# Kernel optimization log

Measured on AMD Instinct MI355X. Metric: run time of the kernel, lower is better.

The kernel has to match this reference:

```python
import jax, jax.numpy as jnp
import numpy as np

NB = 8            # num_blocks
BS = 96           # block_size = hidden_size // num_blocks
HSF = 1           # hidden_size_factor
LAM = 0.01        # sparsity_threshold (softshrink lambda)
FRAC = 1.0        # hard_thresholding_fraction
SCALE = 0.02


def setup_inputs() -> dict:
    key = jax.random.key(0)
    ks = jax.random.split(key, 9)
    B, C, H, W, D = 2, NB * BS, 32, 32, 32
    x = jax.random.normal(ks[0], (B, C, H, W, D), jnp.float32)
    # complex params stored as separate real/imag float arrays (torch.rand on cfloat
    # fills real and imag independently with U[0,1))
    w1r = SCALE * jax.random.uniform(ks[1], (NB, BS, BS * HSF), jnp.float32)
    w1i = SCALE * jax.random.uniform(ks[2], (NB, BS, BS * HSF), jnp.float32)
    w2r = SCALE * jax.random.uniform(ks[3], (NB, BS, BS * HSF), jnp.float32)
    w2i = SCALE * jax.random.uniform(ks[4], (NB, BS, BS * HSF), jnp.float32)
    b1r = SCALE * jax.random.uniform(ks[5], (NB, BS * HSF), jnp.float32)
    b1i = SCALE * jax.random.uniform(ks[6], (NB, BS * HSF), jnp.float32)
    b2r = SCALE * jax.random.uniform(ks[7], (NB, BS), jnp.float32)
    b2i = SCALE * jax.random.uniform(ks[8], (NB, BS), jnp.float32)
    return {"x": x, "w1r": w1r, "w1i": w1i, "w2r": w2r, "w2i": w2i,
            "b1r": b1r, "b1i": b1i, "b2r": b2r, "b2i": b2i}


def _softshrink(v, lam):
    return jnp.sign(v) * jnp.maximum(jnp.abs(v) - lam, 0.0)


def _gelu_c(z):
    # torch GELU applied to view_as_real => separately on real and imag parts
    return jax.nn.gelu(jnp.real(z), approximate=False) + 1j * jax.nn.gelu(jnp.imag(z), approximate=False)


def reference(x, w1r, w1i, w2r, w2i, b1r, b1i, b2r, b2i):
    bias = x
    B, C, H, W, D = x.shape
    w1 = w1r + 1j * w1i
    w2 = w2r + 1j * w2i
    b1 = b1r + 1j * b1i
    b2 = b2r + 1j * b2i

    xf = jnp.fft.rfftn(x.astype(jnp.float32), axes=(-3, -2, -1), norm='ortho')
    Dr = xf.shape[-1]                      # D//2 + 1
    xf = xf.reshape(B, NB, BS, H, W, Dr)

    total_modes = H * W * D // 2 + 1
    kept = min(int(total_modes * FRAC), Dr)  # original slices only the last freq axis
    xk = xf[..., :kept]                      # (B, nb, bs, H, W, kept)

    # block-diagonal complex GEMM 1 + bias, then GELU on real/imag parts
    h1 = jnp.einsum('bnihwd,nio->bnohwd', xk, w1) + b1[None, :, :, None, None, None]
    h1 = _gelu_c(h1)
    # block-diagonal complex GEMM 2 + bias
    h2 = jnp.einsum('bnihwd,nio->bnohwd', h1, w2) + b2[None, :, :, None, None, None]

    # scatter back into full spectrum (zeros beyond kept modes)
    if kept < Dr:
        h2 = jnp.pad(h2, ((0, 0), (0, 0), (0, 0), (0, 0), (0, 0), (0, Dr - kept)))

    # softshrink on real/imag parts
    z = _softshrink(jnp.real(h2), LAM) + 1j * _softshrink(jnp.imag(h2), LAM)
    z = z.reshape(B, C, H, W, Dr)
    out = jnp.fft.irfftn(z, s=(H, W, D), axes=(-3, -2, -1), norm='ortho')
    return out.astype(x.dtype) + bias
```

## Files before the change

kernel.cpp:

```cpp
#include <hip/hip_runtime.h>
#include <math.h>


#define CH    768
#define DR    17
#define PLANE 544
#define NVOL  49152
#define CSTRIDE 17408
#define ORTHO 0.0055242717280199026f
#define TWOPI_32 0.19634954084936207f

typedef __bf16 bf16x8 __attribute__((ext_vector_type(8)));
typedef float  f32x4  __attribute__((ext_vector_type(4)));

#define MFMA __builtin_amdgcn_mfma_f32_16x16x32_bf16

__device__ __forceinline__ float gelu_f(float v) {
    return 0.5f * v * (1.0f + erff(v * 0.7071067811865475f));
}
__device__ __forceinline__ float sshrink(float v) {
    float a = fabsf(v) - 0.01f;
    return a > 0.f ? copysignf(a, v) : 0.f;
}
__device__ __forceinline__ bf16x8 ld8(const __bf16* p) { return *(const bf16x8*)p; }
__device__ __forceinline__ void split2(float v, __bf16* h, __bf16* l) {
    __bf16 hh = (__bf16)v;
    *h = hh;
    *l = (__bf16)(v - (float)hh);
}

__device__ __align__(16) __bf16 gEf[4][1024];
__device__ __align__(16) __bf16 gEb[4][1024];
__device__ __align__(16) __bf16 gC [4][1024];

__global__ void k0_tables() {
    int idx = blockIdx.x * 256 + threadIdx.x;
    if (idx >= 1024) return;
    int c = idx & 31;
    int r = idx >> 5;
    float ang = TWOPI_32 * (float)((r * c) & 31);
    float s, co; sincosf(ang, &s, &co);
    __bf16 h, l;
    split2(co, &h, &l);  gEf[0][idx] = h; gEf[1][idx] = l;
                         gEb[0][idx] = h; gEb[1][idx] = l;
    split2(-s, &h, &l);  gEf[2][idx] = h; gEf[3][idx] = l;
    split2(s, &h, &l);   gEb[2][idx] = h; gEb[3][idx] = l;
    float cf = (c == 0 || c == 16) ? 1.f : (c < DR ? 2.f : 0.f);
    split2(cf * co, &h, &l); gC[0][idx] = h; gC[1][idx] = l;
    split2(-cf * s, &h, &l); gC[2][idx] = h; gC[3][idx] = l;
}

__device__ __align__(16) __bf16 gW1r[73728], gW1i[73728], gW2r[73728], gW2i[73728];

__global__ void k0w(const float* __restrict__ w1r, const float* __restrict__ w1i,
                    const float* __restrict__ w2r, const float* __restrict__ w2i) {
    int idx = blockIdx.x * 256 + threadIdx.x;
    if (idx >= 73728) return;
    int i = idx % 96, no = idx / 96;
    int o = no % 96, n = no / 96;
    int src = n * 9216 + i * 96 + o;
    gW1r[idx] = (__bf16)w1r[src];
    gW1i[idx] = (__bf16)w1i[src];
    gW2r[idx] = (__bf16)w2r[src];
    gW2i[idx] = (__bf16)w2i[src];
}

__global__ __launch_bounds__(256) void k1_fwd_dw(const float* __restrict__ x,
                                                 float2* __restrict__ A) {
    __shared__ __align__(16) __bf16 sArh[32][40], sArl[32][40], sAih[32][40], sAil[32][40];
    const int t = threadIdx.x;
    const int wave = t >> 6, lane = t & 63, row = lane & 15, quad = lane >> 4;
    const int m0 = (wave >> 1) * 16, n0 = (wave & 1) * 16;
    const size_t pb = (size_t)blockIdx.x * 1024;

    const float* xp = x + pb + (size_t)(m0 + row) * 32 + quad * 8;
    f32x4 x0 = *(const f32x4*)xp;
    f32x4 x1 = *(const f32x4*)(xp + 4);
    bf16x8 xh, xl;
    #pragma unroll
    for (int j = 0; j < 4; j++) { __bf16 h = (__bf16)x0[j]; xh[j] = h; xl[j] = (__bf16)(x0[j] - (float)h); }
    #pragma unroll
    for (int j = 0; j < 4; j++) { __bf16 h = (__bf16)x1[j]; xh[4+j] = h; xl[4+j] = (__bf16)(x1[j] - (float)h); }

    {
        const int ed = (n0 + row) * 32 + quad * 8;
        bf16x8 erh = *(const bf16x8*)&gEf[0][ed];
        bf16x8 erl = *(const bf16x8*)&gEf[1][ed];
        bf16x8 eih = *(const bf16x8*)&gEf[2][ed];
        bf16x8 eil = *(const bf16x8*)&gEf[3][ed];
        f32x4 ar = {0.f,0.f,0.f,0.f}, ai = {0.f,0.f,0.f,0.f};
        ar = MFMA(xh, erh, ar, 0,0,0); ar = MFMA(xh, erl, ar, 0,0,0); ar = MFMA(xl, erh, ar, 0,0,0);
        ai = MFMA(xh, eih, ai, 0,0,0); ai = MFMA(xh, eil, ai, 0,0,0); ai = MFMA(xl, eih, ai, 0,0,0);
        #pragma unroll
        for (int r4 = 0; r4 < 4; r4++) {
            int w = m0 + quad * 4 + r4, kd = n0 + row;
            split2(ar[r4], &sArh[kd][w], &sArl[kd][w]);
            split2(ai[r4], &sAih[kd][w], &sAil[kd][w]);
        }
    }
    __syncthreads();
    {
        const int ew = (m0 + row) * 32 + quad * 8;
        bf16x8 frh = *(const bf16x8*)&gEf[0][ew];
        bf16x8 frl = *(const bf16x8*)&gEf[1][ew];
        bf16x8 fih = *(const bf16x8*)&gEf[2][ew];
        bf16x8 fil = *(const bf16x8*)&gEf[3][ew];
        bf16x8 arh = ld8(&sArh[n0 + row][quad * 8]);
        bf16x8 arl = ld8(&sArl[n0 + row][quad * 8]);
        bf16x8 aih = ld8(&sAih[n0 + row][quad * 8]);
        bf16x8 ail = ld8(&sAil[n0 + row][quad * 8]);
        f32x4 rp = {0.f,0.f,0.f,0.f}, rm = {0.f,0.f,0.f,0.f}, im = {0.f,0.f,0.f,0.f};
        rp = MFMA(frh, arh, rp, 0,0,0); rp = MFMA(frh, arl, rp, 0,0,0); rp = MFMA(frl, arh, rp, 0,0,0);
        rm = MFMA(fih, aih, rm, 0,0,0); rm = MFMA(fih, ail, rm, 0,0,0); rm = MFMA(fil, aih, rm, 0,0,0);
        im = MFMA(frh, aih, im, 0,0,0); im = MFMA(frh, ail, im, 0,0,0); im = MFMA(frl, aih, im, 0,0,0);
        im = MFMA(fih, arh, im, 0,0,0); im = MFMA(fih, arl, im, 0,0,0); im = MFMA(fil, arh, im, 0,0,0);
        const size_t ab = (size_t)blockIdx.x * PLANE;
        int kd = n0 + row;
        if (kd < DR) {
            #pragma unroll
            for (int r4 = 0; r4 < 4; r4++) {
                int kw = m0 + quad * 4 + r4;
                A[ab + kw * DR + kd] = make_float2((rp[r4] - rm[r4]) * ORTHO, im[r4] * ORTHO);
            }
        }
    }
}

template <bool INV>
__global__ __launch_bounds__(256) void k2_fft_h(float2* __restrict__ A) {
    __shared__ __align__(16) __bf16 sBr[272][40], sBi[272][40];
    const int t = threadIdx.x;
    const int p0g = blockIdx.x * 272;
    const size_t cb = (size_t)blockIdx.y * CSTRIDE;
    for (int idx = t; idx < 8704; idx += 256) {
        int h = idx / 272, p = idx - h * 272;
        float2 v = A[cb + (size_t)h * PLANE + p0g + p];
        sBr[p][h] = (__bf16)v.x;
        sBi[p][h] = (__bf16)v.y;
    }
    __syncthreads();
    const int wave = t >> 6, lane = t & 63, row = lane & 15, quad = lane >> 4;
    const __bf16* Er = gEf[0];
    const __bf16* Ei = INV ? gEb[2] : gEf[2];
    bf16x8 er0 = *(const bf16x8*)&Er[row * 32 + quad * 8];
    bf16x8 ei0 = *(const bf16x8*)&Ei[row * 32 + quad * 8];
    bf16x8 er1 = *(const bf16x8*)&Er[(16 + row) * 32 + quad * 8];
    bf16x8 ei1 = *(const bf16x8*)&Ei[(16 + row) * 32 + quad * 8];
    for (int j = wave; j < 34; j += 4) {
        int mt = j & 1, nt = j >> 1;
        int m0 = mt * 16, n0 = nt * 16;
        bf16x8 ar = mt ? er1 : er0;
        bf16x8 ai = mt ? ei1 : ei0;
        bf16x8 br = ld8(&sBr[n0 + row][quad * 8]);
        bf16x8 bi = ld8(&sBi[n0 + row][quad * 8]);
        f32x4 rp = {0.f,0.f,0.f,0.f}, rm = {0.f,0.f,0.f,0.f}, im = {0.f,0.f,0.f,0.f};
        rp = MFMA(ar, br, rp, 0, 0, 0);
        rm = MFMA(ai, bi, rm, 0, 0, 0);
        im = MFMA(ar, bi, im, 0, 0, 0);
        im = MFMA(ai, br, im, 0, 0, 0);
        int p = p0g + n0 + row;
        #pragma unroll
        for (int r = 0; r < 4; r++) {
            int kh = m0 + quad * 4 + r;
            A[cb + (size_t)kh * PLANE + p] = make_float2(rp[r] - rm[r], im[r]);
        }
    }
}

__global__ __launch_bounds__(256) void k3_mix(float2* __restrict__ A,
    const float* __restrict__ b1r, const float* __restrict__ b1i,
    const float* __restrict__ b2r, const float* __restrict__ b2i) {
    __shared__ __align__(16) __bf16 sXr[64][104], sXi[64][104];
    const int t = threadIdx.x;
    const int chunk = blockIdx.x, bn = blockIdx.y;
    const int b = bn >> 3, n = bn & 7;
    const size_t base = (size_t)(b * CH + n * 96) * CSTRIDE + chunk * 64;

    for (int idx = t; idx < 6144; idx += 256) {
        int i = idx >> 6, p = idx & 63;
        float2 v = A[base + (size_t)i * CSTRIDE + p];
        sXr[p][i] = (__bf16)v.x;
        sXi[p][i] = (__bf16)v.y;
    }
    __syncthreads();

    const int wave = t >> 6, lane = t & 63, row = lane & 15, quad = lane >> 4;
    const __bf16* W1r = &gW1r[n * 9216];
    const __bf16* W1i = &gW1i[n * 9216];
    const __bf16* W2r = &gW2r[n * 9216];
    const __bf16* W2i = &gW2i[n * 9216];
    float h1s[6][8];

    #pragma unroll
    for (int q = 0; q < 6; q++) {
        int job = wave * 6 + q, mt = job >> 2, nt = job & 3;
        int m0 = mt * 16, p0 = nt * 16;
        f32x4 rp = {0.f,0.f,0.f,0.f}, rm = {0.f,0.f,0.f,0.f}, im = {0.f,0.f,0.f,0.f};
        #pragma unroll
        for (int ks = 0; ks < 3; ks++) {
            int k0 = ks * 32 + quad * 8;
            bf16x8 ar = ld8(&W1r[(m0 + row) * 96 + k0]);
            bf16x8 ai = ld8(&W1i[(m0 + row) * 96 + k0]);
            bf16x8 br = ld8(&sXr[p0 + row][k0]);
            bf16x8 bi = ld8(&sXi[p0 + row][k0]);
            rp = MFMA(ar, br, rp, 0, 0, 0);
            rm = MFMA(ai, bi, rm, 0, 0, 0);
            im = MFMA(ar, bi, im, 0, 0, 0);
            im = MFMA(ai, br, im, 0, 0, 0);
        }
        #pragma unroll
        for (int r = 0; r < 4; r++) {
            int o = m0 + quad * 4 + r;
            float hr = b1r[n * 96 + o] + rp[r] - rm[r];
            float hi = b1i[n * 96 + o] + im[r];
            h1s[q][r]     = gelu_f(hr);
            h1s[q][4 + r] = gelu_f(hi);
        }
    }
    __syncthreads();

    #pragma unroll
    for (int q = 0; q < 6; q++) {
        int job = wave * 6 + q, mt = job >> 2, nt = job & 3;
        int m0 = mt * 16, p0 = nt * 16;
        int p = p0 + row;
        #pragma unroll
        for (int r = 0; r < 4; r++) {
            int o = m0 + quad * 4 + r;
            sXr[p][o] = (__bf16)h1s[q][r];
            sXi[p][o] = (__bf16)h1s[q][4 + r];
        }
    }
    __syncthreads();

    #pragma unroll
    for (int q = 0; q < 6; q++) {
        int job = wave * 6 + q, mt = job >> 2, nt = job & 3;
        int m0 = mt * 16, p0 = nt * 16;
        f32x4 rp = {0.f,0.f,0.f,0.f}, rm = {0.f,0.f,0.f,0.f}, im = {0.f,0.f,0.f,0.f};
        #pragma unroll
        for (int ks = 0; ks < 3; ks++) {
            int k0 = ks * 32 + quad * 8;
            bf16x8 ar = ld8(&W2r[(m0 + row) * 96 + k0]);
            bf16x8 ai = ld8(&W2i[(m0 + row) * 96 + k0]);
            bf16x8 br = ld8(&sXr[p0 + row][k0]);
            bf16x8 bi = ld8(&sXi[p0 + row][k0]);
            rp = MFMA(ar, br, rp, 0, 0, 0);
            rm = MFMA(ai, bi, rm, 0, 0, 0);
            im = MFMA(ar, bi, im, 0, 0, 0);
            im = MFMA(ai, br, im, 0, 0, 0);
        }
        int p = p0 + row;
        #pragma unroll
        for (int r = 0; r < 4; r++) {
            int o = m0 + quad * 4 + r;
            float hr = sshrink(b2r[n * 96 + o] + rp[r] - rm[r]);
            float hi = sshrink(b2i[n * 96 + o] + im[r]);
            A[base + (size_t)o * CSTRIDE + p] = make_float2(hr, hi);
        }
    }
}

__global__ __launch_bounds__(256) void k5_inv_wd(const float2* __restrict__ A,
                                                 const float* __restrict__ x,
                                                 float* __restrict__ out) {
    __shared__ __align__(16) __bf16 sZrh[32][40], sZrl[32][40], sZih[32][40], sZil[32][40];
    const int t = threadIdx.x;
    const int wave = t >> 6, lane = t & 63, row = lane & 15, quad = lane >> 4;
    const int m0 = (wave >> 1) * 16, n0 = (wave & 1) * 16;
    const size_t ab = (size_t)blockIdx.x * PLANE;
    const size_t pb = (size_t)blockIdx.x * 1024;
    const int d = n0 + row;

    float xres[4];
    #pragma unroll
    for (int r4 = 0; r4 < 4; r4++)
        xres[r4] = x[pb + (size_t)(m0 + quad * 4 + r4) * 32 + d];

    for (int idx = t; idx < PLANE; idx += 256) {
        int kw = idx / DR, kd = idx - kw * DR;
        float2 v = A[ab + idx];
        split2(v.x, &sZrh[kd][kw], &sZrl[kd][kw]);
        split2(v.y, &sZih[kd][kw], &sZil[kd][kw]);
    }
    for (int idx = t; idx < 480; idx += 256) {
        int kd = DR + (idx >> 5), kw = idx & 31;
        sZrh[kd][kw] = (__bf16)0.f; sZrl[kd][kw] = (__bf16)0.f;
        sZih[kd][kw] = (__bf16)0.f; sZil[kd][kw] = (__bf16)0.f;
    }
    __syncthreads();

    const int e1 = (m0 + row) * 32 + quad * 8;
    bf16x8 erh = *(const bf16x8*)&gEb[0][e1];
    bf16x8 erl = *(const bf16x8*)&gEb[1][e1];
    bf16x8 eih = *(const bf16x8*)&gEb[2][e1];
    bf16x8 eil = *(const bf16x8*)&gEb[3][e1];
    bf16x8 zrh = ld8(&sZrh[n0 + row][quad * 8]);
    bf16x8 zrl = ld8(&sZrl[n0 + row][quad * 8]);
    bf16x8 zih = ld8(&sZih[n0 + row][quad * 8]);
    bf16x8 zil = ld8(&sZil[n0 + row][quad * 8]);
    f32x4 rp = {0.f,0.f,0.f,0.f}, rm = {0.f,0.f,0.f,0.f}, im = {0.f,0.f,0.f,0.f};
    rp = MFMA(erh, zrh, rp, 0,0,0); rp = MFMA(erh, zrl, rp, 0,0,0); rp = MFMA(erl, zrh, rp, 0,0,0);
    rm = MFMA(eih, zih, rm, 0,0,0); rm = MFMA(eih, zil, rm, 0,0,0); rm = MFMA(eil, zih, rm, 0,0,0);
    im = MFMA(erh, zih, im, 0,0,0); im = MFMA(erh, zil, im, 0,0,0); im = MFMA(erl, zih, im, 0,0,0);
    im = MFMA(eih, zrh, im, 0,0,0); im = MFMA(eih, zrl, im, 0,0,0); im = MFMA(eil, zrh, im, 0,0,0);
    __syncthreads();
    #pragma unroll
    for (int r4 = 0; r4 < 4; r4++) {
        int w = m0 + quad * 4 + r4, kd = n0 + row;
        split2(rp[r4] - rm[r4], &sZrh[w][kd], &sZrl[w][kd]);
        split2(im[r4],          &sZih[w][kd], &sZil[w][kd]);
    }
    __syncthreads();

    const int c2 = d * 32 + quad * 8;
    bf16x8 crh = *(const bf16x8*)&gC[0][c2];
    bf16x8 crl = *(const bf16x8*)&gC[1][c2];
    bf16x8 cih = *(const bf16x8*)&gC[2][c2];
    bf16x8 cil = *(const bf16x8*)&gC[3][c2];
    bf16x8 grh = ld8(&sZrh[m0 + row][quad * 8]);
    bf16x8 grl = ld8(&sZrl[m0 + row][quad * 8]);
    bf16x8 gih = ld8(&sZih[m0 + row][quad * 8]);
    bf16x8 gil = ld8(&sZil[m0 + row][quad * 8]);
    f32x4 acc = {0.f,0.f,0.f,0.f};
    acc = MFMA(grh, crh, acc, 0,0,0); acc = MFMA(grh, crl, acc, 0,0,0); acc = MFMA(grl, crh, acc, 0,0,0);
    acc = MFMA(gih, cih, acc, 0,0,0); acc = MFMA(gih, cil, acc, 0,0,0); acc = MFMA(gil, cih, acc, 0,0,0);
    #pragma unroll
    for (int r4 = 0; r4 < 4; r4++) {
        int w = m0 + quad * 4 + r4;
        out[pb + (size_t)w * 32 + d] = acc[r4] * ORTHO + xres[r4];
    }
}

extern "C" void kernel_launch(void* const* d_in, const int* in_sizes, int n_in,
                              void* d_out, int out_size, void* d_ws, size_t ws_size,
                              hipStream_t stream) {
    const float* x   = (const float*)d_in[0];
    const float* w1r = (const float*)d_in[1];
    const float* w1i = (const float*)d_in[2];
    const float* w2r = (const float*)d_in[3];
    const float* w2i = (const float*)d_in[4];
    const float* b1r = (const float*)d_in[5];
    const float* b1i = (const float*)d_in[6];
    const float* b2r = (const float*)d_in[7];
    const float* b2i = (const float*)d_in[8];
    float* out = (float*)d_out;
    float2* A = (float2*)d_ws;

    k0_tables<<<4, 256, 0, stream>>>();
    k0w<<<288, 256, 0, stream>>>(w1r, w1i, w2r, w2i);
    k1_fwd_dw<<<NVOL, 256, 0, stream>>>(x, A);
    k2_fft_h<false><<<dim3(2, 1536), 256, 0, stream>>>(A);
    k3_mix<<<dim3(272, 16), 256, 0, stream>>>(A, b1r, b1i, b2r, b2i);
    k2_fft_h<true><<<dim3(2, 1536), 256, 0, stream>>>(A);
    k5_inv_wd<<<NVOL, 256, 0, stream>>>(A, x, out);
}
```

Measured before the change: 873.3 us.

## Store intermediate spectrum as bf16 pairs and process two planes per block

Switches the complex spectrum workspace from float2 to packed bf16x2, which halves global traffic in the forward W/D, H-FFT and mixing stages. The inverse H-FFT writes hi/lo bf16 split pairs into a second buffer so the final inverse stage keeps its split-precision accuracy. The forward W/D kernel now handles two planes per block, halving the grid and reusing the DFT table loads. Storing intermediates in bf16 loses precision compared to float and could affect accuracy. The workspace also needs room for the extra low-part buffer.

```diff
diff --git a/kernel.cpp b/kernel.cpp
--- a/kernel.cpp
+++ b/kernel.cpp
@@ -7,10 +7,12 @@
 #define PLANE 544
 #define NVOL  49152
 #define CSTRIDE 17408
+#define NTOT  26738688
 #define ORTHO 0.0055242717280199026f
 #define TWOPI_32 0.19634954084936207f
 
 typedef __bf16 bf16x8 __attribute__((ext_vector_type(8)));
+typedef __bf16 bf16x2 __attribute__((ext_vector_type(2)));
 typedef float  f32x4  __attribute__((ext_vector_type(4)));
 
 #define MFMA __builtin_amdgcn_mfma_f32_16x16x32_bf16
@@ -66,21 +68,24 @@
 }
 
 __global__ __launch_bounds__(256) void k1_fwd_dw(const float* __restrict__ x,
-                                                 float2* __restrict__ A) {
-    __shared__ __align__(16) __bf16 sArh[32][40], sArl[32][40], sAih[32][40], sAil[32][40];
+                                                 bf16x2* __restrict__ A) {
+    __shared__ __align__(16) __bf16 sArh[2][32][40], sArl[2][32][40], sAih[2][32][40], sAil[2][32][40];
     const int t = threadIdx.x;
     const int wave = t >> 6, lane = t & 63, row = lane & 15, quad = lane >> 4;
     const int m0 = (wave >> 1) * 16, n0 = (wave & 1) * 16;
-    const size_t pb = (size_t)blockIdx.x * 1024;
-
-    const float* xp = x + pb + (size_t)(m0 + row) * 32 + quad * 8;
-    f32x4 x0 = *(const f32x4*)xp;
-    f32x4 x1 = *(const f32x4*)(xp + 4);
-    bf16x8 xh, xl;
-    #pragma unroll
-    for (int j = 0; j < 4; j++) { __bf16 h = (__bf16)x0[j]; xh[j] = h; xl[j] = (__bf16)(x0[j] - (float)h); }
-    #pragma unroll
-    for (int j = 0; j < 4; j++) { __bf16 h = (__bf16)x1[j]; xh[4+j] = h; xl[4+j] = (__bf16)(x1[j] - (float)h); }
+    const size_t pb = (size_t)blockIdx.x * 2048;
+
+    bf16x8 xh[2], xl[2];
+    #pragma unroll
+    for (int pl = 0; pl < 2; pl++) {
+        const float* xp = x + pb + pl * 1024 + (size_t)(m0 + row) * 32 + quad * 8;
+        f32x4 x0 = *(const f32x4*)xp;
+        f32x4 x1 = *(const f32x4*)(xp + 4);
+        #pragma unroll
+        for (int j = 0; j < 4; j++) { __bf16 h = (__bf16)x0[j]; xh[pl][j] = h; xl[pl][j] = (__bf16)(x0[j] - (float)h); }
+        #pragma unroll
+        for (int j = 0; j < 4; j++) { __bf16 h = (__bf16)x1[j]; xh[pl][4+j] = h; xl[pl][4+j] = (__bf16)(x1[j] - (float)h); }
+    }
 
     {
         const int ed = (n0 + row) * 32 + quad * 8;
@@ -88,14 +93,17 @@
         bf16x8 erl = *(const bf16x8*)&gEf[1][ed];
         bf16x8 eih = *(const bf16x8*)&gEf[2][ed];
         bf16x8 eil = *(const bf16x8*)&gEf[3][ed];
-        f32x4 ar = {0.f,0.f,0.f,0.f}, ai = {0.f,0.f,0.f,0.f};
-        ar = MFMA(xh, erh, ar, 0,0,0); ar = MFMA(xh, erl, ar, 0,0,0); ar = MFMA(xl, erh, ar, 0,0,0);
-        ai = MFMA(xh, eih, ai, 0,0,0); ai = MFMA(xh, eil, ai, 0,0,0); ai = MFMA(xl, eih, ai, 0,0,0);
-        #pragma unroll
-        for (int r4 = 0; r4 < 4; r4++) {
-            int w = m0 + quad * 4 + r4, kd = n0 + row;
-            split2(ar[r4], &sArh[kd][w], &sArl[kd][w]);
-            split2(ai[r4], &sAih[kd][w], &sAil[kd][w]);
+        #pragma unroll
+        for (int pl = 0; pl < 2; pl++) {
+            f32x4 ar = {0.f,0.f,0.f,0.f}, ai = {0.f,0.f,0.f,0.f};
+            ar = MFMA(xh[pl], erh, ar, 0,0,0); ar = MFMA(xh[pl], erl, ar, 0,0,0); ar = MFMA(xl[pl], erh, ar, 0,0,0);
+            ai = MFMA(xh[pl], eih, ai, 0,0,0); ai = MFMA(xh[pl], eil, ai, 0,0,0); ai = MFMA(xl[pl], eih, ai, 0,0,0);
+            #pragma unroll
+            for (int r4 = 0; r4 < 4; r4++) {
+                int w = m0 + quad * 4 + r4, kd = n0 + row;
+                split2(ar[r4], &sArh[pl][kd][w], &sArl[pl][kd][w]);
+                split2(ai[r4], &sAih[pl][kd][w], &sAil[pl][kd][w]);
+            }
         }
     }
     __syncthreads();
@@ -105,38 +113,44 @@
         bf16x8 frl = *(const bf16x8*)&gEf[1][ew];
         bf16x8 fih = *(const bf16x8*)&gEf[2][ew];
         bf16x8 fil = *(const bf16x8*)&gEf[3][ew];
-        bf16x8 arh = ld8(&sArh[n0 + row][quad * 8]);
-        bf16x8 arl = ld8(&sArl[n0 + row][quad * 8]);
-        bf16x8 aih = ld8(&sAih[n0 + row][quad * 8]);
-        bf16x8 ail = ld8(&sAil[n0 + row][quad * 8]);
-        f32x4 rp = {0.f,0.f,0.f,0.f}, rm = {0.f,0.f,0.f,0.f}, im = {0.f,0.f,0.f,0.f};
-        rp = MFMA(frh, arh, rp, 0,0,0); rp = MFMA(frh, arl, rp, 0,0,0); rp = MFMA(frl, arh, rp, 0,0,0);
-        rm = MFMA(fih, aih, rm, 0,0,0); rm = MFMA(fih, ail, rm, 0,0,0); rm = MFMA(fil, aih, rm, 0,0,0);
-        im = MFMA(frh, aih, im, 0,0,0); im = MFMA(frh, ail, im, 0,0,0); im = MFMA(frl, aih, im, 0,0,0);
-        im = MFMA(fih, arh, im, 0,0,0); im = MFMA(fih, arl, im, 0,0,0); im = MFMA(fil, arh, im, 0,0,0);
-        const size_t ab = (size_t)blockIdx.x * PLANE;
-        int kd = n0 + row;
-        if (kd < DR) {
-            #pragma unroll
-            for (int r4 = 0; r4 < 4; r4++) {
-                int kw = m0 + quad * 4 + r4;
-                A[ab + kw * DR + kd] = make_float2((rp[r4] - rm[r4]) * ORTHO, im[r4] * ORTHO);
+        const int kd = n0 + row;
+        #pragma unroll
+        for (int pl = 0; pl < 2; pl++) {
+            bf16x8 arh = ld8(&sArh[pl][n0 + row][quad * 8]);
+            bf16x8 arl = ld8(&sArl[pl][n0 + row][quad * 8]);
+            bf16x8 aih = ld8(&sAih[pl][n0 + row][quad * 8]);
+            bf16x8 ail = ld8(&sAil[pl][n0 + row][quad * 8]);
+            f32x4 rp = {0.f,0.f,0.f,0.f}, rm = {0.f,0.f,0.f,0.f}, im = {0.f,0.f,0.f,0.f};
+            rp = MFMA(frh, arh, rp, 0,0,0); rp = MFMA(frh, arl, rp, 0,0,0); rp = MFMA(frl, arh, rp, 0,0,0);
+            rm = MFMA(fih, aih, rm, 0,0,0); rm = MFMA(fih, ail, rm, 0,0,0); rm = MFMA(fil, aih, rm, 0,0,0);
+            im = MFMA(frh, aih, im, 0,0,0); im = MFMA(frh, ail, im, 0,0,0); im = MFMA(frl, aih, im, 0,0,0);
+            im = MFMA(fih, arh, im, 0,0,0); im = MFMA(fih, arl, im, 0,0,0); im = MFMA(fil, arh, im, 0,0,0);
+            if (kd < DR) {
+                const size_t ab = ((size_t)blockIdx.x * 2 + pl) * PLANE;
+                #pragma unroll
+                for (int r4 = 0; r4 < 4; r4++) {
+                    int kw = m0 + quad * 4 + r4;
+                    bf16x2 o;
+                    o.x = (__bf16)((rp[r4] - rm[r4]) * ORTHO);
+                    o.y = (__bf16)(im[r4] * ORTHO);
+                    A[ab + kw * DR + kd] = o;
+                }
             }
         }
     }
 }
 
 template <bool INV>
-__global__ __launch_bounds__(256) void k2_fft_h(float2* __restrict__ A) {
+__global__ __launch_bounds__(256) void k2_fft_h(bf16x2* __restrict__ A) {
     __shared__ __align__(16) __bf16 sBr[272][40], sBi[272][40];
     const int t = threadIdx.x;
     const int p0g = blockIdx.x * 272;
     const size_t cb = (size_t)blockIdx.y * CSTRIDE;
     for (int idx = t; idx < 8704; idx += 256) {
         int h = idx / 272, p = idx - h * 272;
-        float2 v = A[cb + (size_t)h * PLANE + p0g + p];
-        sBr[p][h] = (__bf16)v.x;
-        sBi[p][h] = (__bf16)v.y;
+        bf16x2 v = A[cb + (size_t)h * PLANE + p0g + p];
+        sBr[p][h] = v.x;
+        sBi[p][h] = v.y;
     }
     __syncthreads();
     const int wave = t >> 6, lane = t & 63, row = lane & 15, quad = lane >> 4;
@@ -162,12 +176,26 @@
         #pragma unroll
         for (int r = 0; r < 4; r++) {
             int kh = m0 + quad * 4 + r;
-            A[cb + (size_t)kh * PLANE + p] = make_float2(rp[r] - rm[r], im[r]);
-        }
-    }
-}
-
-__global__ __launch_bounds__(256) void k3_mix(float2* __restrict__ A,
+            size_t oidx = cb + (size_t)kh * PLANE + p;
+            if (!INV) {
+                bf16x2 o;
+                o.x = (__bf16)(rp[r] - rm[r]);
+                o.y = (__bf16)im[r];
+                A[oidx] = o;
+            } else {
+                __bf16 rh, rl, ih, il;
+                split2(rp[r] - rm[r], &rh, &rl);
+                split2(im[r], &ih, &il);
+                bf16x2 oh; oh.x = rh; oh.y = ih;
+                bf16x2 ol; ol.x = rl; ol.y = il;
+                A[oidx] = oh;
+                A[NTOT + oidx] = ol;
+            }
+        }
+    }
+}
+
+__global__ __launch_bounds__(256) void k3_mix(bf16x2* __restrict__ A,
     const float* __restrict__ b1r, const float* __restrict__ b1i,
     const float* __restrict__ b2r, const float* __restrict__ b2i) {
     __shared__ __align__(16) __bf16 sXr[64][104], sXi[64][104];
@@ -178,9 +206,9 @@
 
     for (int idx = t; idx < 6144; idx += 256) {
         int i = idx >> 6, p = idx & 63;
-        float2 v = A[base + (size_t)i * CSTRIDE + p];
-        sXr[p][i] = (__bf16)v.x;
-        sXi[p][i] = (__bf16)v.y;
+        bf16x2 v = A[base + (size_t)i * CSTRIDE + p];
+        sXr[p][i] = v.x;
+        sXi[p][i] = v.y;
     }
     __syncthreads();
 
@@ -254,14 +282,15 @@
         #pragma unroll
         for (int r = 0; r < 4; r++) {
             int o = m0 + quad * 4 + r;
-            float hr = sshrink(b2r[n * 96 + o] + rp[r] - rm[r]);
-            float hi = sshrink(b2i[n * 96 + o] + im[r]);
-            A[base + (size_t)o * CSTRIDE + p] = make_float2(hr, hi);
-        }
-    }
-}
-
-__global__ __launch_bounds__(256) void k5_inv_wd(const float2* __restrict__ A,
+            bf16x2 oV;
+            oV.x = (__bf16)sshrink(b2r[n * 96 + o] + rp[r] - rm[r]);
+            oV.y = (__bf16)sshrink(b2i[n * 96 + o] + im[r]);
+            A[base + (size_t)o * CSTRIDE + p] = oV;
+        }
+    }
+}
+
+__global__ __launch_bounds__(256) void k5_inv_wd(const bf16x2* __restrict__ A,
                                                  const float* __restrict__ x,
                                                  float* __restrict__ out) {
     __shared__ __align__(16) __bf16 sZrh[32][40], sZrl[32][40], sZih[32][40], sZil[32][40];
@@ -279,9 +308,10 @@
 
     for (int idx = t; idx < PLANE; idx += 256) {
         int kw = idx / DR, kd = idx - kw * DR;
-        float2 v = A[ab + idx];
-        split2(v.x, &sZrh[kd][kw], &sZrl[kd][kw]);
-        split2(v.y, &sZih[kd][kw], &sZil[kd][kw]);
+        bf16x2 h = A[ab + idx];
+        bf16x2 l = A[NTOT + ab + idx];
+        sZrh[kd][kw] = h.x; sZrl[kd][kw] = l.x;
+        sZih[kd][kw] = h.y; sZil[kd][kw] = l.y;
     }
     for (int idx = t; idx < 480; idx += 256) {
         int kd = DR + (idx >> 5), kw = idx & 31;
@@ -345,11 +375,11 @@
     const float* b2r = (const float*)d_in[7];
     const float* b2i = (const float*)d_in[8];
     float* out = (float*)d_out;
-    float2* A = (float2*)d_ws;
+    bf16x2* A = (bf16x2*)d_ws;
 
     k0_tables<<<4, 256, 0, stream>>>();
     k0w<<<288, 256, 0, stream>>>(w1r, w1i, w2r, w2i);
-    k1_fwd_dw<<<NVOL, 256, 0, stream>>>(x, A);
+    k1_fwd_dw<<<NVOL / 2, 256, 0, stream>>>(x, A);
     k2_fft_h<false><<<dim3(2, 1536), 256, 0, stream>>>(A);
     k3_mix<<<dim3(272, 16), 256, 0, stream>>>(A, b1r, b1i, b2r, b2i);
     k2_fft_h<true><<<dim3(2, 1536), 256, 0, stream>>>(A);
```

New measurement: 847.6 us. -2.9%, faster.
